# Kernel tuning notes

Measured on AMD Instinct MI355X. Metric: run time of the kernel, lower is better.

The kernel has to match this reference:

```python
import jax, jax.numpy as jnp
import numpy as np

B, T_CACHE, N_STATE, N_HEAD = 128, 448, 1280, 20
HEAD_DIM = N_STATE // N_HEAD


def setup_inputs() -> dict:
    key = jax.random.key(0)
    ks = jax.random.split(key, 10)
    s = 1.0 / np.sqrt(N_STATE)
    return {
        "x": jax.random.normal(ks[0], (B, 1, N_STATE), jnp.float32),
        "k_cache": jax.random.normal(ks[1], (B, T_CACHE, N_STATE), jnp.float32),
        "v_cache": jax.random.normal(ks[2], (B, T_CACHE, N_STATE), jnp.float32),
        "mask": jnp.zeros((1, T_CACHE), jnp.float32),
        "Wq": jax.random.normal(ks[3], (N_STATE, N_STATE), jnp.float32) * s,
        "bq": jax.random.normal(ks[4], (N_STATE,), jnp.float32) * s,
        "Wk": jax.random.normal(ks[5], (N_STATE, N_STATE), jnp.float32) * s,
        "Wv": jax.random.normal(ks[6], (N_STATE, N_STATE), jnp.float32) * s,
        "bv": jax.random.normal(ks[7], (N_STATE,), jnp.float32) * s,
        "Wo": jax.random.normal(ks[8], (N_STATE, N_STATE), jnp.float32) * s,
        "bo": jax.random.normal(ks[9], (N_STATE,), jnp.float32) * s,
    }


def reference(x, k_cache, v_cache, mask, Wq, bq, Wk, Wv, bv, Wo, bo):
    b, q_len, n_state = x.shape  # q_len == 1 in loop (streaming) mode
    h, d = N_HEAD, n_state // N_HEAD

    # Q/K/V projections (Whisper: key has no bias)
    q = x @ Wq + bq                         # [B, 1, n_state]
    k = x @ Wk                              # [B, 1, n_state]
    v = x @ Wv + bv                         # [B, 1, n_state]

    # streaming KV-cache shift-and-append
    k_cache = jnp.concatenate([k_cache[:, 1:, :], k], axis=1)  # [B, T, n_state]
    v_cache = jnp.concatenate([v_cache[:, 1:, :], v], axis=1)

    t = k_cache.shape[1]
    scale = d ** (-0.25)
    qh = q.reshape(b, q_len, h, d).transpose(0, 2, 1, 3) * scale   # [B, H, q, d]
    kh = k_cache.reshape(b, t, h, d).transpose(0, 2, 3, 1) * scale  # [B, H, d, T]
    vh = v_cache.reshape(b, t, h, d).transpose(0, 2, 1, 3)          # [B, H, T, d]

    qk = jnp.matmul(qh, kh) + mask          # [B, H, q, T]
    qk = qk.astype(jnp.float32)
    w = jax.nn.softmax(qk, axis=-1).astype(qh.dtype)
    wv = jnp.matmul(w, vh)                  # [B, H, q, d]
    wv = wv.transpose(0, 2, 1, 3).reshape(b, q_len, n_state)

    out = wv @ Wo + bo                      # [B, q, n_state]
    return out, k_cache, v_cache
```

## Files before the change

kernel.cpp:

```cpp
#include <hip/hip_runtime.h>
#include <cstddef>

#define NSTATE 1280
#define TCACHE 448
#define NBATCH 128
#define NHEAD  20
#define HDIM   64
#define NT     8
#define RPC    (TCACHE / NT)
#define KSPLIT 4
#define KRANGE (NSTATE / KSPLIT)

typedef float f4 __attribute__((ext_vector_type(4)));
typedef float f32x4 __attribute__((ext_vector_type(4)));
typedef short bf16x8 __attribute__((ext_vector_type(8)));
typedef unsigned short u16;
typedef unsigned short u16x8 __attribute__((ext_vector_type(8)));

__device__ __forceinline__ u16 f2bf(float f) {
    unsigned u = __builtin_bit_cast(unsigned, f);
    u += 0x7fff + ((u >> 16) & 1);
    return (u16)(u >> 16);
}

__device__ __forceinline__ void mfma_partial_body(
    const float* __restrict__ A, const float* __restrict__ W,
    float* __restrict__ P)
{
    __shared__ u16 As[128][40];
    __shared__ u16 Bs[64][40];
    const int tid = threadIdx.x;
    const int n0 = blockIdx.x * 64;
    const int kb = blockIdx.y * KRANGE;
    const int w = tid >> 6, l = tid & 63;
    const int la = l & 15, kg = l >> 4;
    const int arow = tid >> 1, akh = (tid & 1) << 4;
    const int bkr = tid >> 3, bnc = (tid & 7) << 3;
    f32x4 acc[8] = {};

    for (int ks = 0; ks < KRANGE; ks += 32) {
        {
            const float* src = A + (size_t)arow * NSTATE + kb + ks + akh;
            float4 v0 = *(const float4*)(src);
            float4 v1 = *(const float4*)(src + 4);
            float4 v2 = *(const float4*)(src + 8);
            float4 v3 = *(const float4*)(src + 12);
            u16x8 w0, w1;
            w0[0]=f2bf(v0.x); w0[1]=f2bf(v0.y); w0[2]=f2bf(v0.z); w0[3]=f2bf(v0.w);
            w0[4]=f2bf(v1.x); w0[5]=f2bf(v1.y); w0[6]=f2bf(v1.z); w0[7]=f2bf(v1.w);
            w1[0]=f2bf(v2.x); w1[1]=f2bf(v2.y); w1[2]=f2bf(v2.z); w1[3]=f2bf(v2.w);
            w1[4]=f2bf(v3.x); w1[5]=f2bf(v3.y); w1[6]=f2bf(v3.z); w1[7]=f2bf(v3.w);
            *(u16x8*)&As[arow][akh]     = w0;
            *(u16x8*)&As[arow][akh + 8] = w1;
        }
        {
            const float* src = W + (size_t)(kb + ks + bkr) * NSTATE + n0 + bnc;
            float4 b0 = *(const float4*)(src);
            float4 b1 = *(const float4*)(src + 4);
            Bs[bnc + 0][bkr] = f2bf(b0.x); Bs[bnc + 1][bkr] = f2bf(b0.y);
            Bs[bnc + 2][bkr] = f2bf(b0.z); Bs[bnc + 3][bkr] = f2bf(b0.w);
            Bs[bnc + 4][bkr] = f2bf(b1.x); Bs[bnc + 5][bkr] = f2bf(b1.y);
            Bs[bnc + 6][bkr] = f2bf(b1.z); Bs[bnc + 7][bkr] = f2bf(b1.w);
        }
        __syncthreads();
        const bf16x8 bf = *(const bf16x8*)&Bs[w * 16 + la][kg * 8];
        #pragma unroll
        for (int mf = 0; mf < 8; ++mf) {
            bf16x8 af = *(const bf16x8*)&As[mf * 16 + la][kg * 8];
            acc[mf] = __builtin_amdgcn_mfma_f32_16x16x32_bf16(af, bf, acc[mf], 0, 0, 0);
        }
        __syncthreads();
    }
    const int col = n0 + w * 16 + la;
    #pragma unroll
    for (int mf = 0; mf < 8; ++mf)
        #pragma unroll
        for (int j = 0; j < 4; ++j)
            P[(size_t)(mf * 16 + kg * 4 + j) * NSTATE + col] = acc[mf][j];
}

__global__ void __launch_bounds__(256) proj_mfma_kernel(
    const float* __restrict__ x,
    const float* __restrict__ Wq, const float* __restrict__ Wk,
    const float* __restrict__ Wv, float* __restrict__ pp)
{
    const int z = blockIdx.z;
    const float* W = (z == 0) ? Wq : (z == 1) ? Wk : Wv;
    mfma_partial_body(x, W,
        pp + (size_t)(z * KSPLIT + blockIdx.y) * NBATCH * NSTATE);
}

__global__ void __launch_bounds__(256) proj_reduce_kernel(
    const float* __restrict__ pp, const float* __restrict__ bq,
    const float* __restrict__ bv, float* __restrict__ q_ws,
    float* __restrict__ kout, float* __restrict__ vout)
{
    const int mat = blockIdx.y;
    const size_t idx = ((size_t)blockIdx.x * 256 + threadIdx.x) * 4;
    const int b = (int)(idx / NSTATE), col = (int)(idx % NSTATE);
    float4 v = make_float4(0.f, 0.f, 0.f, 0.f);
    #pragma unroll
    for (int c = 0; c < KSPLIT; ++c) {
        float4 a = *(const float4*)(pp + (size_t)(mat * KSPLIT + c) * NBATCH * NSTATE + idx);
        v.x += a.x; v.y += a.y; v.z += a.z; v.w += a.w;
    }
    if (mat == 0) {
        float4 bb = *(const float4*)(bq + col);
        v.x = (v.x + bb.x) * 0.125f; v.y = (v.y + bb.y) * 0.125f;
        v.z = (v.z + bb.z) * 0.125f; v.w = (v.w + bb.w) * 0.125f;
        *(float4*)(q_ws + idx) = v;
    } else if (mat == 1) {
        *(float4*)(kout + ((size_t)b * TCACHE + TCACHE - 1) * NSTATE + col) = v;
    } else {
        float4 bb = *(const float4*)(bv + col);
        v.x += bb.x; v.y += bb.y; v.z += bb.z; v.w += bb.w;
        *(float4*)(vout + ((size_t)b * TCACHE + TCACHE - 1) * NSTATE + col) = v;
    }
}

__global__ void __launch_bounds__(320) fused_stream_kernel(
    const float* __restrict__ kin, const float* __restrict__ vin,
    const float* __restrict__ q_ws, const float* __restrict__ mask,
    float* __restrict__ kout, float* __restrict__ vout,
    float* __restrict__ pvp, float* __restrict__ m_ws, float* __restrict__ s_ws)
{
    const int tc = blockIdx.x, b = blockIdx.y;
    const int tid = threadIdx.x;
    const int h = tid >> 4, l = tid & 15;
    const int col = tid << 2;
    const size_t base = (size_t)b * TCACHE * NSTATE;
    const bool last = (tc == NT - 1);
    const int nrows = last ? RPC - 1 : RPC;
    const size_t RSTEP = (size_t)NT * NSTATE;

    __shared__ float sc[NHEAD][RPC];

    const float4 q4 = *(const float4*)(q_ws + (size_t)b * NSTATE + col);
    const float* ksrc = kin + base + (size_t)(tc + 1) * NSTATE + col;
    const float* vsrc = vin + base + (size_t)(tc + 1) * NSTATE + col;
    float* kdst = kout + base + (size_t)tc * NSTATE + col;
    float* vdst = vout + base + (size_t)tc * NSTATE + col;

    {
        int r = 0;
        for (; r + 8 <= nrows; r += 8) {
            f4 kb[8];
            #pragma unroll
            for (int j = 0; j < 8; ++j)
                kb[j] = __builtin_nontemporal_load((const f4*)(ksrc + (size_t)(r + j) * RSTEP));
            #pragma unroll
            for (int j = 0; j < 8; ++j)
                __builtin_nontemporal_store(kb[j], (f4*)(kdst + (size_t)(r + j) * RSTEP));
            #pragma unroll
            for (int j = 0; j < 8; ++j) {
                float p = kb[j][0]*q4.x + kb[j][1]*q4.y + kb[j][2]*q4.z + kb[j][3]*q4.w;
                p += __shfl_xor(p, 1); p += __shfl_xor(p, 2);
                p += __shfl_xor(p, 4); p += __shfl_xor(p, 8);
                if (l == 0) sc[h][r + j] = p + mask[tc + NT * (r + j)];
            }
        }
        for (; r < nrows; ++r) {
            f4 kv = __builtin_nontemporal_load((const f4*)(ksrc + (size_t)r * RSTEP));
            __builtin_nontemporal_store(kv, (f4*)(kdst + (size_t)r * RSTEP));
            float p = kv[0]*q4.x + kv[1]*q4.y + kv[2]*q4.z + kv[3]*q4.w;
            p += __shfl_xor(p, 1); p += __shfl_xor(p, 2);
            p += __shfl_xor(p, 4); p += __shfl_xor(p, 8);
            if (l == 0) sc[h][r] = p + mask[tc + NT * r];
        }
        if (last) {
            const f4 kv = *(const f4*)(kout + base + (size_t)(TCACHE-1) * NSTATE + col);
            float p = kv[0]*q4.x + kv[1]*q4.y + kv[2]*q4.z + kv[3]*q4.w;
            p += __shfl_xor(p, 1); p += __shfl_xor(p, 2);
            p += __shfl_xor(p, 4); p += __shfl_xor(p, 8);
            if (l == 0) sc[h][RPC - 1] = p + mask[TCACHE - 1];
        }
    }
    __syncthreads();

    {
        float v[4];
        float m = -1e30f;
        #pragma unroll
        for (int j = 0; j < 4; ++j) {
            int r = l + 16 * j;
            v[j] = (r < RPC) ? sc[h][r] : -1e30f;
            m = fmaxf(m, v[j]);
        }
        #pragma unroll
        for (int d = 1; d <= 8; d <<= 1) m = fmaxf(m, __shfl_xor(m, d));
        float s = 0.f;
        #pragma unroll
        for (int j = 0; j < 4; ++j) {
            v[j] = __expf(v[j] - m);
            s += v[j];
        }
        #pragma unroll
        for (int d = 1; d <= 8; d <<= 1) s += __shfl_xor(s, d);
        __syncthreads();
        #pragma unroll
        for (int j = 0; j < 4; ++j) {
            int r = l + 16 * j;
            if (r < RPC) sc[h][r] = v[j];
        }
        if (l == 0) {
            m_ws[((size_t)b * NT + tc) * NHEAD + h] = m;
            s_ws[((size_t)b * NT + tc) * NHEAD + h] = s;
        }
    }
    __syncthreads();

    float ax = 0.f, ay = 0.f, az = 0.f, aw = 0.f;
    {
        int r = 0;
        for (; r + 8 <= nrows; r += 8) {
            f4 vb[8];
            #pragma unroll
            for (int j = 0; j < 8; ++j)
                vb[j] = __builtin_nontemporal_load((const f4*)(vsrc + (size_t)(r + j) * RSTEP));
            #pragma unroll
            for (int j = 0; j < 8; ++j)
                __builtin_nontemporal_store(vb[j], (f4*)(vdst + (size_t)(r + j) * RSTEP));
            #pragma unroll
            for (int j = 0; j < 8; ++j) {
                const float w = sc[h][r + j];
                ax = fmaf(w, vb[j][0], ax); ay = fmaf(w, vb[j][1], ay);
                az = fmaf(w, vb[j][2], az); aw = fmaf(w, vb[j][3], aw);
            }
        }
        for (; r < nrows; ++r) {
            f4 vv = __builtin_nontemporal_load((const f4*)(vsrc + (size_t)r * RSTEP));
            __builtin_nontemporal_store(vv, (f4*)(vdst + (size_t)r * RSTEP));
            const float w = sc[h][r];
            ax = fmaf(w, vv[0], ax); ay = fmaf(w, vv[1], ay);
            az = fmaf(w, vv[2], az); aw = fmaf(w, vv[3], aw);
        }
        if (last) {
            const f4 vv = *(const f4*)(vout + base + (size_t)(TCACHE-1) * NSTATE + col);
            const float w = sc[h][RPC - 1];
            ax = fmaf(w, vv[0], ax); ay = fmaf(w, vv[1], ay);
            az = fmaf(w, vv[2], az); aw = fmaf(w, vv[3], aw);
        }
    }
    *(float4*)(pvp + ((size_t)b * NT + tc) * NSTATE + col) =
        make_float4(ax, ay, az, aw);
}

__global__ void __launch_bounds__(256) combine_kernel(
    const float* __restrict__ pvp, const float* __restrict__ m_ws,
    const float* __restrict__ s_ws, float* __restrict__ wv_ws)
{
    const size_t idx = ((size_t)blockIdx.x * 256 + threadIdx.x) * 4;
    const int b = (int)(idx / NSTATE), col = (int)(idx % NSTATE);
    const int h = col >> 6;

    float m[NT], s[NT];
    float M = -1e30f;
    #pragma unroll
    for (int c = 0; c < NT; ++c) {
        m[c] = m_ws[((size_t)b * NT + c) * NHEAD + h];
        s[c] = s_ws[((size_t)b * NT + c) * NHEAD + h];
        M = fmaxf(M, m[c]);
    }
    float S = 0.f;
    float f[NT];
    #pragma unroll
    for (int c = 0; c < NT; ++c) { f[c] = __expf(m[c] - M); S += s[c] * f[c]; }
    const float inv = 1.0f / S;

    float4 acc = make_float4(0.f, 0.f, 0.f, 0.f);
    #pragma unroll
    for (int c = 0; c < NT; ++c) {
        const float w = f[c] * inv;
        float4 a = *(const float4*)(pvp + ((size_t)b * NT + c) * NSTATE + col);
        acc.x = fmaf(w, a.x, acc.x); acc.y = fmaf(w, a.y, acc.y);
        acc.z = fmaf(w, a.z, acc.z); acc.w = fmaf(w, a.w, acc.w);
    }
    *(float4*)(wv_ws + idx) = acc;
}

__global__ void __launch_bounds__(256) outproj_mfma_kernel(
    const float* __restrict__ wv, const float* __restrict__ Wo,
    float* __restrict__ po)
{
    mfma_partial_body(wv, Wo, po + (size_t)blockIdx.y * NBATCH * NSTATE);
}

__global__ void __launch_bounds__(256) out_reduce_kernel(
    const float* __restrict__ po, const float* __restrict__ bo,
    float* __restrict__ out)
{
    const size_t idx = ((size_t)blockIdx.x * 256 + threadIdx.x) * 4;
    const int col = (int)(idx % NSTATE);
    float4 s = *(const float4*)(bo + col);
    #pragma unroll
    for (int c = 0; c < KSPLIT; ++c) {
        float4 a = *(const float4*)(po + (size_t)c * NBATCH * NSTATE + idx);
        s.x += a.x; s.y += a.y; s.z += a.z; s.w += a.w;
    }
    *(float4*)(out + idx) = s;
}

extern "C" void kernel_launch(void* const* d_in, const int* in_sizes, int n_in,
                              void* d_out, int out_size, void* d_ws, size_t ws_size,
                              hipStream_t stream)
{
    const float* x       = (const float*)d_in[0];
    const float* k_cache = (const float*)d_in[1];
    const float* v_cache = (const float*)d_in[2];
    const float* mask    = (const float*)d_in[3];
    const float* Wq      = (const float*)d_in[4];
    const float* bq      = (const float*)d_in[5];
    const float* Wk      = (const float*)d_in[6];
    const float* Wv      = (const float*)d_in[7];
    const float* bv      = (const float*)d_in[8];
    const float* Wo      = (const float*)d_in[9];
    const float* bo      = (const float*)d_in[10];

    float* out  = (float*)d_out;
    float* kout = out + (size_t)NBATCH * NSTATE;
    float* vout = kout + (size_t)NBATCH * TCACHE * NSTATE;

    float* ws     = (float*)d_ws;
    float* q_ws   = ws;
    float* pvp_ws = q_ws  + (size_t)NBATCH * NSTATE;
    float* m_ws   = pvp_ws + (size_t)NBATCH * NT * NSTATE;
    float* s_ws   = m_ws  + (size_t)NBATCH * NT * NHEAD;
    float* wv_ws  = s_ws  + (size_t)NBATCH * NT * NHEAD;
    float* pp_ws  = wv_ws + (size_t)NBATCH * NSTATE;
    float* po_ws  = pp_ws + (size_t)3 * KSPLIT * NBATCH * NSTATE;

    proj_mfma_kernel<<<dim3(20, KSPLIT, 3), 256, 0, stream>>>(x, Wq, Wk, Wv, pp_ws);
    proj_reduce_kernel<<<dim3(160, 3), 256, 0, stream>>>(pp_ws, bq, bv,
                                                         q_ws, kout, vout);
    fused_stream_kernel<<<dim3(NT, NBATCH), 320, 0, stream>>>(
        k_cache, v_cache, q_ws, mask, kout, vout, pvp_ws, m_ws, s_ws);
    combine_kernel<<<dim3(160), 256, 0, stream>>>(pvp_ws, m_ws, s_ws, wv_ws);
    outproj_mfma_kernel<<<dim3(20, KSPLIT), 256, 0, stream>>>(wv_ws, Wo, po_ws);
    out_reduce_kernel<<<dim3(160), 256, 0, stream>>>(po_ws, bo, out);
}
```

Baseline: 261.2 us.

## Fuse K and V streaming into one pass with max-free softmax accumulation

The attention-streaming kernel now loads, copies and consumes K and V rows together in a single loop. Each row's exponentiated score is accumulated straight into the weighted V sum, which removes the shared-memory score buffer, the block-wide syncs and the separate max/exp phase. The combine kernel simply sums the per-chunk partial exps and accumulators. Dropping the max subtraction removes the m_ws workspace and its rescaling work, but exp can overflow when attention logits are large.

```diff
diff --git a/kernel.cpp b/kernel.cpp
--- a/kernel.cpp
+++ b/kernel.cpp
@@ -122,7 +122,7 @@
     const float* __restrict__ kin, const float* __restrict__ vin,
     const float* __restrict__ q_ws, const float* __restrict__ mask,
     float* __restrict__ kout, float* __restrict__ vout,
-    float* __restrict__ pvp, float* __restrict__ m_ws, float* __restrict__ s_ws)
+    float* __restrict__ pvp, float* __restrict__ s_ws)
 {
     const int tc = blockIdx.x, b = blockIdx.y;
     const int tid = threadIdx.x;
@@ -133,148 +133,87 @@
     const int nrows = last ? RPC - 1 : RPC;
     const size_t RSTEP = (size_t)NT * NSTATE;
 
-    __shared__ float sc[NHEAD][RPC];
-
-    const float4 q4 = *(const float4*)(q_ws + (size_t)b * NSTATE + col);
+    const f4 q4 = *(const f4*)(q_ws + (size_t)b * NSTATE + col);
     const float* ksrc = kin + base + (size_t)(tc + 1) * NSTATE + col;
     const float* vsrc = vin + base + (size_t)(tc + 1) * NSTATE + col;
     float* kdst = kout + base + (size_t)tc * NSTATE + col;
     float* vdst = vout + base + (size_t)tc * NSTATE + col;
 
-    {
-        int r = 0;
-        for (; r + 8 <= nrows; r += 8) {
-            f4 kb[8];
-            #pragma unroll
-            for (int j = 0; j < 8; ++j)
-                kb[j] = __builtin_nontemporal_load((const f4*)(ksrc + (size_t)(r + j) * RSTEP));
-            #pragma unroll
-            for (int j = 0; j < 8; ++j)
-                __builtin_nontemporal_store(kb[j], (f4*)(kdst + (size_t)(r + j) * RSTEP));
-            #pragma unroll
-            for (int j = 0; j < 8; ++j) {
-                float p = kb[j][0]*q4.x + kb[j][1]*q4.y + kb[j][2]*q4.z + kb[j][3]*q4.w;
-                p += __shfl_xor(p, 1); p += __shfl_xor(p, 2);
-                p += __shfl_xor(p, 4); p += __shfl_xor(p, 8);
-                if (l == 0) sc[h][r + j] = p + mask[tc + NT * (r + j)];
-            }
-        }
-        for (; r < nrows; ++r) {
-            f4 kv = __builtin_nontemporal_load((const f4*)(ksrc + (size_t)r * RSTEP));
-            __builtin_nontemporal_store(kv, (f4*)(kdst + (size_t)r * RSTEP));
-            float p = kv[0]*q4.x + kv[1]*q4.y + kv[2]*q4.z + kv[3]*q4.w;
+    float s = 0.f;
+    f4 acc = {0.f, 0.f, 0.f, 0.f};
+
+    int r = 0;
+    for (; r + 4 <= nrows; r += 4) {
+        f4 kb[4], vb[4];
+        #pragma unroll
+        for (int j = 0; j < 4; ++j)
+            kb[j] = __builtin_nontemporal_load((const f4*)(ksrc + (size_t)(r + j) * RSTEP));
+        #pragma unroll
+        for (int j = 0; j < 4; ++j)
+            vb[j] = __builtin_nontemporal_load((const f4*)(vsrc + (size_t)(r + j) * RSTEP));
+        #pragma unroll
+        for (int j = 0; j < 4; ++j)
+            __builtin_nontemporal_store(kb[j], (f4*)(kdst + (size_t)(r + j) * RSTEP));
+        #pragma unroll
+        for (int j = 0; j < 4; ++j)
+            __builtin_nontemporal_store(vb[j], (f4*)(vdst + (size_t)(r + j) * RSTEP));
+        #pragma unroll
+        for (int j = 0; j < 4; ++j) {
+            float p = kb[j][0]*q4[0] + kb[j][1]*q4[1] + kb[j][2]*q4[2] + kb[j][3]*q4[3];
             p += __shfl_xor(p, 1); p += __shfl_xor(p, 2);
             p += __shfl_xor(p, 4); p += __shfl_xor(p, 8);
-            if (l == 0) sc[h][r] = p + mask[tc + NT * r];
-        }
-        if (last) {
-            const f4 kv = *(const f4*)(kout + base + (size_t)(TCACHE-1) * NSTATE + col);
-            float p = kv[0]*q4.x + kv[1]*q4.y + kv[2]*q4.z + kv[3]*q4.w;
-            p += __shfl_xor(p, 1); p += __shfl_xor(p, 2);
-            p += __shfl_xor(p, 4); p += __shfl_xor(p, 8);
-            if (l == 0) sc[h][RPC - 1] = p + mask[TCACHE - 1];
-        }
-    }
-    __syncthreads();
-
-    {
-        float v[4];
-        float m = -1e30f;
-        #pragma unroll
-        for (int j = 0; j < 4; ++j) {
-            int r = l + 16 * j;
-            v[j] = (r < RPC) ? sc[h][r] : -1e30f;
-            m = fmaxf(m, v[j]);
-        }
-        #pragma unroll
-        for (int d = 1; d <= 8; d <<= 1) m = fmaxf(m, __shfl_xor(m, d));
-        float s = 0.f;
-        #pragma unroll
-        for (int j = 0; j < 4; ++j) {
-            v[j] = __expf(v[j] - m);
-            s += v[j];
-        }
-        #pragma unroll
-        for (int d = 1; d <= 8; d <<= 1) s += __shfl_xor(s, d);
-        __syncthreads();
-        #pragma unroll
-        for (int j = 0; j < 4; ++j) {
-            int r = l + 16 * j;
-            if (r < RPC) sc[h][r] = v[j];
-        }
-        if (l == 0) {
-            m_ws[((size_t)b * NT + tc) * NHEAD + h] = m;
-            s_ws[((size_t)b * NT + tc) * NHEAD + h] = s;
-        }
-    }
-    __syncthreads();
-
-    float ax = 0.f, ay = 0.f, az = 0.f, aw = 0.f;
-    {
-        int r = 0;
-        for (; r + 8 <= nrows; r += 8) {
-            f4 vb[8];
-            #pragma unroll
-            for (int j = 0; j < 8; ++j)
-                vb[j] = __builtin_nontemporal_load((const f4*)(vsrc + (size_t)(r + j) * RSTEP));
-            #pragma unroll
-            for (int j = 0; j < 8; ++j)
-                __builtin_nontemporal_store(vb[j], (f4*)(vdst + (size_t)(r + j) * RSTEP));
-            #pragma unroll
-            for (int j = 0; j < 8; ++j) {
-                const float w = sc[h][r + j];
-                ax = fmaf(w, vb[j][0], ax); ay = fmaf(w, vb[j][1], ay);
-                az = fmaf(w, vb[j][2], az); aw = fmaf(w, vb[j][3], aw);
-            }
-        }
-        for (; r < nrows; ++r) {
-            f4 vv = __builtin_nontemporal_load((const f4*)(vsrc + (size_t)r * RSTEP));
-            __builtin_nontemporal_store(vv, (f4*)(vdst + (size_t)r * RSTEP));
-            const float w = sc[h][r];
-            ax = fmaf(w, vv[0], ax); ay = fmaf(w, vv[1], ay);
-            az = fmaf(w, vv[2], az); aw = fmaf(w, vv[3], aw);
-        }
-        if (last) {
-            const f4 vv = *(const f4*)(vout + base + (size_t)(TCACHE-1) * NSTATE + col);
-            const float w = sc[h][RPC - 1];
-            ax = fmaf(w, vv[0], ax); ay = fmaf(w, vv[1], ay);
-            az = fmaf(w, vv[2], az); aw = fmaf(w, vv[3], aw);
-        }
-    }
-    *(float4*)(pvp + ((size_t)b * NT + tc) * NSTATE + col) =
-        make_float4(ax, ay, az, aw);
+            const float e = __expf(p + mask[tc + NT * (r + j)]);
+            s += e;
+            acc += vb[j] * e;
+        }
+    }
+    for (; r < nrows; ++r) {
+        f4 kv = __builtin_nontemporal_load((const f4*)(ksrc + (size_t)r * RSTEP));
+        f4 vv = __builtin_nontemporal_load((const f4*)(vsrc + (size_t)r * RSTEP));
+        __builtin_nontemporal_store(kv, (f4*)(kdst + (size_t)r * RSTEP));
+        __builtin_nontemporal_store(vv, (f4*)(vdst + (size_t)r * RSTEP));
+        float p = kv[0]*q4[0] + kv[1]*q4[1] + kv[2]*q4[2] + kv[3]*q4[3];
+        p += __shfl_xor(p, 1); p += __shfl_xor(p, 2);
+        p += __shfl_xor(p, 4); p += __shfl_xor(p, 8);
+        const float e = __expf(p + mask[tc + NT * r]);
+        s += e;
+        acc += vv * e;
+    }
+    if (last) {
+        const f4 kv = *(const f4*)(kout + base + (size_t)(TCACHE-1) * NSTATE + col);
+        const f4 vv = *(const f4*)(vout + base + (size_t)(TCACHE-1) * NSTATE + col);
+        float p = kv[0]*q4[0] + kv[1]*q4[1] + kv[2]*q4[2] + kv[3]*q4[3];
+        p += __shfl_xor(p, 1); p += __shfl_xor(p, 2);
+        p += __shfl_xor(p, 4); p += __shfl_xor(p, 8);
+        const float e = __expf(p + mask[TCACHE - 1]);
+        s += e;
+        acc += vv * e;
+    }
+
+    if (l == 0) s_ws[((size_t)b * NT + tc) * NHEAD + h] = s;
+    *(f4*)(pvp + ((size_t)b * NT + tc) * NSTATE + col) = acc;
 }
 
 __global__ void __launch_bounds__(256) combine_kernel(
-    const float* __restrict__ pvp, const float* __restrict__ m_ws,
-    const float* __restrict__ s_ws, float* __restrict__ wv_ws)
+    const float* __restrict__ pvp, const float* __restrict__ s_ws,
+    float* __restrict__ wv_ws)
 {
     const size_t idx = ((size_t)blockIdx.x * 256 + threadIdx.x) * 4;
     const int b = (int)(idx / NSTATE), col = (int)(idx % NSTATE);
     const int h = col >> 6;
 
-    float m[NT], s[NT];
-    float M = -1e30f;
+    float S = 0.f;
+    #pragma unroll
+    for (int c = 0; c < NT; ++c) S += s_ws[((size_t)b * NT + c) * NHEAD + h];
+    const float inv = 1.0f / S;
+
+    float4 acc = make_float4(0.f, 0.f, 0.f, 0.f);
     #pragma unroll
     for (int c = 0; c < NT; ++c) {
-        m[c] = m_ws[((size_t)b * NT + c) * NHEAD + h];
-        s[c] = s_ws[((size_t)b * NT + c) * NHEAD + h];
-        M = fmaxf(M, m[c]);
-    }
-    float S = 0.f;
-    float f[NT];
-    #pragma unroll
-    for (int c = 0; c < NT; ++c) { f[c] = __expf(m[c] - M); S += s[c] * f[c]; }
-    const float inv = 1.0f / S;
-
-    float4 acc = make_float4(0.f, 0.f, 0.f, 0.f);
-    #pragma unroll
-    for (int c = 0; c < NT; ++c) {
-        const float w = f[c] * inv;
         float4 a = *(const float4*)(pvp + ((size_t)b * NT + c) * NSTATE + col);
-        acc.x = fmaf(w, a.x, acc.x); acc.y = fmaf(w, a.y, acc.y);
-        acc.z = fmaf(w, a.z, acc.z); acc.w = fmaf(w, a.w, acc.w);
-    }
+        acc.x += a.x; acc.y += a.y; acc.z += a.z; acc.w += a.w;
+    }
+    acc.x *= inv; acc.y *= inv; acc.z *= inv; acc.w *= inv;
     *(float4*)(wv_ws + idx) = acc;
 }
 
@@ -323,8 +262,7 @@
     float* ws     = (float*)d_ws;
     float* q_ws   = ws;
     float* pvp_ws = q_ws  + (size_t)NBATCH * NSTATE;
-    float* m_ws   = pvp_ws + (size_t)NBATCH * NT * NSTATE;
-    float* s_ws   = m_ws  + (size_t)NBATCH * NT * NHEAD;
+    float* s_ws   = pvp_ws + (size_t)NBATCH * NT * NSTATE;
     float* wv_ws  = s_ws  + (size_t)NBATCH * NT * NHEAD;
     float* pp_ws  = wv_ws + (size_t)NBATCH * NSTATE;
     float* po_ws  = pp_ws + (size_t)3 * KSPLIT * NBATCH * NSTATE;
@@ -333,8 +271,8 @@
     proj_reduce_kernel<<<dim3(160, 3), 256, 0, stream>>>(pp_ws, bq, bv,
                                                          q_ws, kout, vout);
     fused_stream_kernel<<<dim3(NT, NBATCH), 320, 0, stream>>>(
-        k_cache, v_cache, q_ws, mask, kout, vout, pvp_ws, m_ws, s_ws);
-    combine_kernel<<<dim3(160), 256, 0, stream>>>(pvp_ws, m_ws, s_ws, wv_ws);
+        k_cache, v_cache, q_ws, mask, kout, vout, pvp_ws, s_ws);
+    combine_kernel<<<dim3(160), 256, 0, stream>>>(pvp_ws, s_ws, wv_ws);
     outproj_mfma_kernel<<<dim3(20, KSPLIT), 256, 0, stream>>>(wv_ws, Wo, po_ws);
     out_reduce_kernel<<<dim3(160), 256, 0, stream>>>(po_ws, bo, out);
 }
```

Measured after the change: 266.5 us. +2.0%, slower.
